# Kernel optimization log

Hardware: AMD Instinct MI355X
Metric: run time of the kernel (lower is better)

Reference implementation:

```python
import jax, jax.numpy as jnp
import numpy as np

D, H, HD, DEPTH, V, L, BOS = 128, 16, 8, 16, 17, 1024, 16

def _ln(x, s, b):
    m = jnp.mean(x, -1, keepdims=True)
    v = jnp.mean((x - m) ** 2, -1, keepdims=True)
    return (x - m) * jax.lax.rsqrt(v + 1e-5) * s + b

def _transformer(tok, emb, pos, layers, lnf_s, lnf_b, head_w, head_b):
    # tok: [B,S] int tokens. GPT-style pre-LN decoder, causal attention.
    B, S = tok.shape
    h = emb[tok] + pos[:S]
    causal = jnp.tril(jnp.ones((S, S), dtype=bool))
    inv_sqrt = np.float32(1.0 / np.sqrt(HD))
    def layer(h, p):
        ln1_s, ln1_b, wqkv, bqkv, wo, bo, ln2_s, ln2_b, w1, b1, w2, b2 = p
        x = _ln(h, ln1_s, ln1_b)
        qkv = x @ wqkv + bqkv  # [B,S,3D]
        q, k, v = jnp.split(qkv, 3, axis=-1)
        q = q.reshape(B, S, H, HD)
        k = k.reshape(B, S, H, HD)
        v = v.reshape(B, S, H, HD)
        att = jnp.einsum('bshd,bthd->bhst', q, k) * inv_sqrt
        att = jax.nn.softmax(jnp.where(causal, att, -1e9), axis=-1)
        o = jnp.einsum('bhst,bthd->bshd', att, v).reshape(B, S, D)
        h = h + o @ wo + bo
        x = _ln(h, ln2_s, ln2_b)
        h = h + jax.nn.gelu(x @ w1 + b1) @ w2 + b2
        return h, None
    h, _ = jax.lax.scan(layer, h, layers)
    return _ln(h, lnf_s, lnf_b) @ head_w + head_b  # [B,S,V]

def setup_inputs() -> dict:
    key = jax.random.key(0)
    ks = jax.random.split(key, 8)
    s = 0.02
    return {
        'tokens': jax.random.randint(ks[0], (1, L), 0, BOS, dtype=jnp.int32),
        'emb': jax.random.normal(ks[1], (V, D), jnp.float32) * s,
        'pos': jax.random.normal(ks[2], (L, D), jnp.float32) * s,
        'ln1_s': jnp.ones((DEPTH, D)), 'ln1_b': jnp.zeros((DEPTH, D)),
        'wqkv': jax.random.normal(ks[3], (DEPTH, D, 3 * D), jnp.float32) * s,
        'bqkv': jnp.zeros((DEPTH, 3 * D)),
        'wo': jax.random.normal(ks[4], (DEPTH, D, D), jnp.float32) * s,
        'bo': jnp.zeros((DEPTH, D)),
        'ln2_s': jnp.ones((DEPTH, D)), 'ln2_b': jnp.zeros((DEPTH, D)),
        'w1': jax.random.normal(ks[5], (DEPTH, D, 4 * D), jnp.float32) * s,
        'b1': jnp.zeros((DEPTH, 4 * D)),
        'w2': jax.random.normal(ks[6], (DEPTH, 4 * D, D), jnp.float32) * s,
        'b2': jnp.zeros((DEPTH, D)),
        'lnf_s': jnp.ones((D,)), 'lnf_b': jnp.zeros((D,)),
        'head_w': jax.random.normal(ks[7], (D, V), jnp.float32) * s,
        'head_b': jnp.zeros((V,)),
    }

def reference(tokens, emb, pos, ln1_s, ln1_b, wqkv, bqkv, wo, bo, ln2_s, ln2_b, w1, b1, w2, b2, lnf_s, lnf_b, head_w, head_b):
    layers = (ln1_s, ln1_b, wqkv, bqkv, wo, bo, ln2_s, ln2_b, w1, b1, w2, b2)
    tf = lambda t: _transformer(t, emb, pos, layers, lnf_s, lnf_b, head_w, head_b)
    # BOS-pad (pad value == num_embeddings == 16), as in F.pad(latent,(1,0),value=16)
    lat = jnp.concatenate([jnp.full((1, 1), BOS, jnp.int32), tokens.astype(jnp.int32)], axis=1)  # [1,1025]
    # likelihood pass: next-token log-prob of each latent token
    logits = tf(lat[:, :L])                               # [1,1024,V]
    logp = jax.nn.log_softmax(logits, axis=-1)
    ll = jnp.take_along_axis(logp, lat[:, 1:, None], axis=-1)[..., 0]  # [1,1024]
    mask = ll[0] < jnp.quantile(ll, 0.03)
    # token-healing loop: per masked position, rerun transformer, argmax (BOS excluded)
    def body(i, lat):
        def heal(lat):
            lg = tf(lat[:, :L])  # causal => position i-1 equals prefix-run logits
            row = jax.lax.dynamic_index_in_dim(lg, i - 1, axis=1, keepdims=False)[0]  # [V]
            probs = jax.nn.softmax(row).at[BOS].set(0.0)
            return lat.at[:, i].set(jnp.argmax(probs).astype(jnp.int32))
        return jax.lax.cond(mask[i - 1], heal, lambda l: l, lat)
    lat = jax.lax.fori_loop(1, L + 1, body, lat)
    out_logits = tf(lat[:, :L])  # logits over healed sequence (float output)
    return (out_logits, lat[:, 1:])
```

## Files before the change

kernel.cpp:

```cpp
#include <hip/hip_runtime.h>
#include <math.h>

#define D 128
#define NLAYER 16
#define V 17
#define L 1024
#define BOSX 16
#define NWG 256
#define NT 512

struct P {
  const int* tokens;
  const float *emb, *pos, *ln1_s, *ln1_b, *wqkv, *bqkv, *wo, *bo;
  const float *ln2_s, *ln2_b, *w1, *b1, *w2, *b2, *lnf_s, *lnf_b, *hw, *hb;
  float *kc, *vc, *ll_;
  int *lat, *heal_row, *barc, *done, *heals_done, *prog;
  float *logits, *out_tok;
};

__device__ __forceinline__ void stUf(float* p, float v) {
  __hip_atomic_store(p, v, __ATOMIC_RELAXED, __HIP_MEMORY_SCOPE_SYSTEM);
}
__device__ __forceinline__ int ldUi(const int* p) {
  return __hip_atomic_load((int*)p, __ATOMIC_RELAXED, __HIP_MEMORY_SCOPE_SYSTEM);
}
__device__ __forceinline__ void stUi(int* p, int v) {
  __hip_atomic_store(p, v, __ATOMIC_RELAXED, __HIP_MEMORY_SCOPE_SYSTEM);
}

__device__ __forceinline__ void barFull(int* cnt, int& b) {
  asm volatile("s_waitcnt vmcnt(0)" ::: "memory");
  __syncthreads();
  if (threadIdx.x == 0) {
    __threadfence();
    __hip_atomic_fetch_add(cnt, 1, __ATOMIC_RELAXED, __HIP_MEMORY_SCOPE_AGENT);
    int tgt = (b + 1) * NWG;
    while (__hip_atomic_load(cnt, __ATOMIC_RELAXED, __HIP_MEMORY_SCOPE_AGENT) < tgt)
      __builtin_amdgcn_s_sleep(8);
    __threadfence();
  }
  b += 1;
  __syncthreads();
}

__device__ __forceinline__ float geluf(float a) {
  float cgv = 0.7978845608028654f * (a + 0.044715f * a * a * a);
  cgv = fminf(fmaxf(cgv, -15.f), 15.f);
  float e = __expf(2.f * cgv);
  return 0.5f * a * (1.f + (e - 1.f) / (e + 1.f));
}

__device__ void lnorm(const float* __restrict__ s, const float* __restrict__ b,
                      const float* in, float* out, float* red) {
  int t = threadIdx.x;
  float v = (t < D) ? in[t] : 0.f;
  float sm = v;
#pragma unroll
  for (int o = 32; o; o >>= 1) sm += __shfl_xor(sm, o, 64);
  if (t < D && (t & 63) == 0) red[t >> 6] = sm;
  __syncthreads();
  float mean = (red[0] + red[1]) * (1.f / 128.f);
  float d = (t < D) ? (v - mean) : 0.f;
  float vs = d * d;
#pragma unroll
  for (int o = 32; o; o >>= 1) vs += __shfl_xor(vs, o, 64);
  if (t < D && (t & 63) == 0) red[2 + (t >> 6)] = vs;
  __syncthreads();
  float rstd = rsqrtf((red[2] + red[3]) * (1.f / 128.f) + 1e-5f);
  if (t < D) out[t] = d * rstd * s[t] + b[t];
  __syncthreads();
}

template <bool HEAL>
__device__ void qkvPub(const P& p, int l, int row, int split, const float* x, float* qrow) {
  int t = threadIdx.x;
  if (t < 384) {
    const float* w = p.wqkv + (size_t)l * D * 384 + t;
    float a = 0.f;
#pragma unroll 8
    for (int d = 0; d < D; ++d) a += x[d] * w[d * 384];
    a += p.bqkv[l * 384 + t];
    float* kcl = p.kc + (size_t)l * L * D + (size_t)row * D;
    float* vcl = p.vc + (size_t)l * L * D + (size_t)row * D;
    if (t < 128) qrow[t] = a;
    else if (t < 256) { if (HEAL) stUf(&kcl[t - 128], a); else kcl[t - 128] = a; }
    else              { if (HEAL) stUf(&vcl[t - 256], a); else vcl[t - 256] = a; }
  }
  if (HEAL) {
    asm volatile("s_waitcnt vmcnt(0)" ::: "memory");
    __syncthreads();
    if (t == 0) {
      int* dl = p.done + l * L;
      if (row - 1 >= split)
        while (ldUi(&dl[row - 1]) < 1) __builtin_amdgcn_s_sleep(1);
      stUi(&dl[row], 1);
    }
    __syncthreads();
  } else {
    __syncthreads();
  }
}

__device__ void attnProjFFN(const P& p, int row, int l,
                            float* hrow, const float* qrow,
                            float* oS, float* xnS, float* fS, float* padS, float* redS) {
  int t = threadIdx.x;
  const float* kcl = p.kc + (size_t)l * L * D;
  const float* vcl = p.vc + (size_t)l * L * D;
  int head = t >> 5, lane = t & 31;
  const float* qh = qrow + head * 8;
  float q0=qh[0],q1=qh[1],q2=qh[2],q3=qh[3],q4=qh[4],q5=qh[5],q6=qh[6],q7=qh[7];
  float sum = 0.f, a0=0,a1=0,a2=0,a3=0,a4=0,a5=0,a6=0,a7=0;
#pragma unroll 2
  for (int key = lane; key <= row; key += 32) {
    const float4* kp = (const float4*)(kcl + (size_t)key * D + head * 8);
    float4 k0 = kp[0], k1 = kp[1];
    float sc = q0*k0.x+q1*k0.y+q2*k0.z+q3*k0.w+q4*k1.x+q5*k1.y+q6*k1.z+q7*k1.w;
    float pr = __expf(sc * 0.35355339059327376f);
    const float4* vp = (const float4*)(vcl + (size_t)key * D + head * 8);
    float4 v0 = vp[0], v1 = vp[1];
    sum += pr;
    a0+=pr*v0.x; a1+=pr*v0.y; a2+=pr*v0.z; a3+=pr*v0.w;
    a4+=pr*v1.x; a5+=pr*v1.y; a6+=pr*v1.z; a7+=pr*v1.w;
  }
#pragma unroll
  for (int o = 1; o < 32; o <<= 1) {
    sum += __shfl_xor(sum, o, 32);
    a0 += __shfl_xor(a0, o, 32); a1 += __shfl_xor(a1, o, 32);
    a2 += __shfl_xor(a2, o, 32); a3 += __shfl_xor(a3, o, 32);
    a4 += __shfl_xor(a4, o, 32); a5 += __shfl_xor(a5, o, 32);
    a6 += __shfl_xor(a6, o, 32); a7 += __shfl_xor(a7, o, 32);
  }
  if (lane == 0) {
    float inv = 1.f / sum;
    oS[head*8+0]=a0*inv; oS[head*8+1]=a1*inv; oS[head*8+2]=a2*inv; oS[head*8+3]=a3*inv;
    oS[head*8+4]=a4*inv; oS[head*8+5]=a5*inv; oS[head*8+6]=a6*inv; oS[head*8+7]=a7*inv;
  }
  __syncthreads();
  {
    int col = t & 127, seg = t >> 7;
    const float* wp = p.wo + (size_t)l * D * D + col;
    float acc = 0.f;
    int d0 = seg * 32;
#pragma unroll 8
    for (int d = d0; d < d0 + 32; ++d) acc += oS[d] * wp[d * D];
    padS[t] = acc;
  }
  __syncthreads();
  if (t < D) hrow[t] += padS[t] + padS[t+128] + padS[t+256] + padS[t+384] + p.bo[l * D + t];
  __syncthreads();
  lnorm(p.ln2_s + l * D, p.ln2_b + l * D, hrow, xnS, redS);
  {
    const float* w1p = p.w1 + (size_t)l * D * 512 + t;
    float acc = 0.f;
#pragma unroll 8
    for (int d = 0; d < D; ++d) acc += xnS[d] * w1p[d * 512];
    fS[t] = geluf(acc + p.b1[l * 512 + t]);
  }
  __syncthreads();
  {
    int col = t & 127, seg = t >> 7;
    const float* w2p = p.w2 + (size_t)l * 512 * D + col;
    float acc = 0.f;
    int d0 = seg * 128;
#pragma unroll 8
    for (int d = d0; d < d0 + 128; ++d) acc += fS[d] * w2p[d * D];
    padS[t] = acc;
  }
  __syncthreads();
  if (t < D) hrow[t] += padS[t] + padS[t+128] + padS[t+256] + padS[t+384] + p.b2[l * D + t];
  __syncthreads();
}

template <bool HEAL>
__device__ void headRow(const P& p, int row, float* hrow,
                        float* xnS, float* redS, float* padS, float* oS) {
  lnorm(p.lnf_s, p.lnf_b, hrow, xnS, redS);
  int t = threadIdx.x;
  if (t < V * 8) {
    int col = t >> 3, seg = t & 7;
    float acc = 0.f;
    int d0 = seg * 16;
#pragma unroll
    for (int d = d0; d < d0 + 16; ++d) acc += xnS[d] * p.hw[d * V + col];
    padS[t] = acc;
  }
  __syncthreads();
  if (t < V) {
    float a = padS[t*8]+padS[t*8+1]+padS[t*8+2]+padS[t*8+3]
            + padS[t*8+4]+padS[t*8+5]+padS[t*8+6]+padS[t*8+7] + p.hb[t];
    oS[t] = a;
    if (HEAL) stUf(&p.logits[row * V + t], a);
    else      p.logits[row * V + t] = a;
  }
  __syncthreads();
}

__global__ void kInit(const int* __restrict__ tokens, int* __restrict__ lat,
                      int* __restrict__ barc, int* __restrict__ done,
                      int* __restrict__ hd) {
  int i = blockIdx.x * blockDim.x + threadIdx.x;
  if (i == 0) stUi(lat, BOSX);
  if (i < L) stUi(lat + i + 1, tokens[i]);
  if (i < 64) stUi(barc + i, 0);
  if (i < 16) stUi(hd + i, 0);
  if (i < NLAYER * L) stUi(done + i, 0);
}

__global__ void __launch_bounds__(NT, 1) kMega(P p) {
  __shared__ float hS[4][D];
  __shared__ float qS[4][D];
  __shared__ float xnS[D];
  __shared__ float oS[D];
  __shared__ float fS[512];
  __shared__ float padS[512];
  __shared__ float redS[16];
  __shared__ float sortS[L];
  __shared__ int cntS[NT + 1];
  int wg = blockIdx.x, t = threadIdx.x;
  int b = 0;
  int* cnt = p.barc;

  for (int i = 0; i < 4; ++i) {
    int row = wg + i * NWG;
    int tok = p.lat[row];
    if (t < D) hS[i][t] = p.emb[tok * D + t] + p.pos[row * D + t];
    __syncthreads();
    lnorm(p.ln1_s, p.ln1_b, hS[i], xnS, redS);
    qkvPub<false>(p, 0, row, 0, xnS, qS[i]);
  }
  barFull(cnt, b);
  for (int l = 0; l < NLAYER; ++l) {
    for (int i = 0; i < 4; ++i) {
      int row = wg + i * NWG;
      attnProjFFN(p, row, l, hS[i], qS[i], oS, xnS, fS, padS, redS);
      if (l < NLAYER - 1) {
        lnorm(p.ln1_s + (l+1)*D, p.ln1_b + (l+1)*D, hS[i], xnS, redS);
        qkvPub<false>(p, l + 1, row, 0, xnS, qS[i]);
      } else {
        headRow<false>(p, row, hS[i], xnS, redS, padS, oS);
      }
    }
    barFull(cnt, b);
  }

  {
    int gid = wg * NT + t;
    if (gid < L) {
      float r[V];
#pragma unroll
      for (int v = 0; v < V; ++v) r[v] = p.logits[gid * V + v];
      float m = r[0];
#pragma unroll
      for (int v = 1; v < V; ++v) m = fmaxf(m, r[v]);
      float s = 0.f;
#pragma unroll
      for (int v = 0; v < V; ++v) s += expf(r[v] - m);
      p.ll_[gid] = r[p.lat[gid + 1]] - (m + logf(s));
    }
  }
  barFull(cnt, b);

  if (wg == 0) {
    for (int i = t; i < L; i += NT) sortS[i] = p.ll_[i];
    __syncthreads();
    for (int ksz = 2; ksz <= L; ksz <<= 1) {
      for (int j = ksz >> 1; j; j >>= 1) {
        for (int i = t; i < L; i += NT) {
          int l2 = i ^ j;
          if (l2 > i) {
            bool up = ((i & ksz) == 0);
            float a = sortS[i], bb = sortS[l2];
            if ((a > bb) == up) { sortS[i] = bb; sortS[l2] = a; }
          }
        }
        __syncthreads();
      }
    }
    if (t == 0) {
      double frac = 0.03 * 1023.0 - 30.0;
      redS[0] = (float)((double)sortS[30] + frac * ((double)sortS[31] - (double)sortS[30]));
    }
    __syncthreads();
    float val = redS[0];
    float lv0 = p.ll_[t * 2], lv1 = p.ll_[t * 2 + 1];
    int loc[2], cc = 0;
    if (lv0 < val) loc[cc++] = t * 2;
    if (lv1 < val) loc[cc++] = t * 2 + 1;
    cntS[t] = cc;
    __syncthreads();
    if (t == 0) {
      int run = 0;
      for (int i = 0; i < NT; ++i) { int c2 = cntS[i]; cntS[i] = run; run += c2; }
      cntS[NT] = run;
    }
    __syncthreads();
    int base = cntS[t];
    for (int j = 0; j < cc; ++j)
      if (base + j < 31) p.heal_row[base + j] = loc[j];
    __syncthreads();
    if (t == 0) {
      int c = cntS[NT]; if (c > 31) c = 31;
      p.heal_row[31] = c;
      stUi(p.heals_done, 1);
      if (c > 0) {
        int r0 = p.heal_row[0];
        int best = 0; float bv = p.logits[r0 * V];
        for (int v = 1; v < BOSX; ++v) {
          float x = p.logits[r0 * V + v];
          if (x > bv) { bv = x; best = v; }
        }
        stUi(&p.lat[r0 + 1], best);
      }
    }
  }
  barFull(cnt, b);

  int c = p.heal_row[31];
  int split = (c > 0) ? (p.heal_row[0] + 1) : L;
  for (int r = split + wg; r < L; r += NWG) {
    int nh = 0, hk = -1;
    bool firstRow = false;
    for (int j = 0; j < c; ++j) {
      nh += (p.heal_row[j] < r) ? 1 : 0;
      if (j >= 1 && p.heal_row[j] == r) hk = j;
      if (p.heal_row[j] == r - 1) firstRow = true;
    }
    {
      int pfi = (wg * 7) % 96;
      for (;;) {
        if (t == 0) { cntS[0] = ldUi(p.heals_done); cntS[1] = ldUi(p.prog); }
        __syncthreads();
        if (cntS[0] >= nh) break;
        int pl = (cntS[1] + 1) & 15;
        float sink = 0.f;
#pragma unroll
        for (int j2 = 0; j2 < 4; ++j2) {
          int ch = pfi + j2; if (ch >= 96) ch -= 96;
          const float* basep; int off;
          if (ch < 24)      { basep = p.wqkv + (size_t)pl * D * 384; off = ch * 2048; }
          else if (ch < 32) { basep = p.wo   + (size_t)pl * D * D;   off = (ch - 24) * 2048; }
          else if (ch < 64) { basep = p.w1   + (size_t)pl * D * 512; off = (ch - 32) * 2048; }
          else              { basep = p.w2   + (size_t)pl * 512 * D; off = (ch - 64) * 2048; }
          float4 v = *(const float4*)(basep + off + t * 4);
          sink += v.x + v.y + v.z + v.w;
        }
        asm volatile("" :: "v"(sink));
        pfi += 4; if (pfi >= 96) pfi -= 96;
        __syncthreads();
      }
      if (t == 0) cntS[0] = ldUi(&p.lat[r]);
      __syncthreads();
    }
    int tok = cntS[0];
    if (t < D) hS[0][t] = p.emb[tok * D + t] + p.pos[r * D + t];
    __syncthreads();
    lnorm(p.ln1_s, p.ln1_b, hS[0], xnS, redS);
    qkvPub<true>(p, 0, r, split, xnS, qS[0]);
    for (int l = 0; l < NLAYER; ++l) {
      if (firstRow && t == 0) stUi(p.prog, l);
      attnProjFFN(p, r, l, hS[0], qS[0], oS, xnS, fS, padS, redS);
      if (l < NLAYER - 1) {
        lnorm(p.ln1_s + (l+1)*D, p.ln1_b + (l+1)*D, hS[0], xnS, redS);
        qkvPub<true>(p, l + 1, r, split, xnS, qS[0]);
      } else {
        headRow<true>(p, r, hS[0], xnS, redS, padS, oS);
      }
    }
    if (hk >= 0 && t == 0) {
      int best = 0; float bv = oS[0];
      for (int v = 1; v < BOSX; ++v)
        if (oS[v] > bv) { bv = oS[v]; best = v; }
      stUi(&p.lat[r + 1], best);
      asm volatile("s_waitcnt vmcnt(0)" ::: "memory");
      stUi(p.heals_done, hk + 1);
    }
  }

  barFull(cnt, b);

  {
    int gid = wg * NT + t;
    if (gid < L) p.out_tok[gid] = (float)ldUi(&p.lat[gid + 1]);
  }
}

extern "C" void kernel_launch(void* const* d_in, const int* in_sizes, int n_in,
                              void* d_out, int out_size, void* d_ws, size_t ws_size,
                              hipStream_t stream) {
  P prm;
  prm.tokens = (const int*)d_in[0];
  prm.emb    = (const float*)d_in[1];
  prm.pos    = (const float*)d_in[2];
  prm.ln1_s  = (const float*)d_in[3];
  prm.ln1_b  = (const float*)d_in[4];
  prm.wqkv   = (const float*)d_in[5];
  prm.bqkv   = (const float*)d_in[6];
  prm.wo     = (const float*)d_in[7];
  prm.bo     = (const float*)d_in[8];
  prm.ln2_s  = (const float*)d_in[9];
  prm.ln2_b  = (const float*)d_in[10];
  prm.w1     = (const float*)d_in[11];
  prm.b1     = (const float*)d_in[12];
  prm.w2     = (const float*)d_in[13];
  prm.b2     = (const float*)d_in[14];
  prm.lnf_s  = (const float*)d_in[15];
  prm.lnf_b  = (const float*)d_in[16];
  prm.hw     = (const float*)d_in[17];
  prm.hb     = (const float*)d_in[18];

  float* ws = (float*)d_ws;
  prm.kc   = ws;
  prm.vc   = prm.kc + (size_t)NLAYER*L*D;
  prm.ll_  = prm.vc + (size_t)NLAYER*L*D;
  prm.lat        = (int*)(prm.ll_ + L);
  prm.heal_row   = prm.lat + 1032;
  prm.barc       = prm.heal_row + 32;
  prm.done       = prm.barc + 64;
  prm.heals_done = prm.done + NLAYER * L;
  prm.prog       = prm.heals_done + 8;

  prm.logits  = (float*)d_out;
  prm.out_tok = prm.logits + L * V;

  kInit<<<64, 256, 0, stream>>>(prm.tokens, prm.lat, prm.barc, prm.done, prm.heals_done);

  void* args[] = { &prm };
  (void)hipLaunchCooperativeKernel((const void*)kMega, dim3(NWG), dim3(NT), args, 0, stream);
}
```

Measured before the change: 18.54 ms.

## Extend idle-wait prefetch to KV cache, spin-only for lead row, deeper unroll

Workgroups that are waiting on heals now also touch KV-cache blocks of the upcoming layer in their prefetch loop, in addition to the weight matrices, and prefetch six chunks per iteration instead of four. The workgroup that computes the row right after a healed position now spins with a sleep on thread 0 instead of issuing prefetch loads, so it does not contend for bandwidth on the critical path. Matvec unroll factors for the QKV, W1 and W2 loops go from 8 to 16. The goal is to keep next-layer data warm in L2 and cut latency on the serial healing chain. The cost is extra memory traffic from the waiting workgroups and higher register pressure from the deeper unrolling.

```diff
diff --git a/kernel.cpp b/kernel.cpp
--- a/kernel.cpp
+++ b/kernel.cpp
@@ -77,7 +77,7 @@
   if (t < 384) {
     const float* w = p.wqkv + (size_t)l * D * 384 + t;
     float a = 0.f;
-#pragma unroll 8
+#pragma unroll 16
     for (int d = 0; d < D; ++d) a += x[d] * w[d * 384];
     a += p.bqkv[l * 384 + t];
     float* kcl = p.kc + (size_t)l * L * D + (size_t)row * D;
@@ -153,7 +153,7 @@
   {
     const float* w1p = p.w1 + (size_t)l * D * 512 + t;
     float acc = 0.f;
-#pragma unroll 8
+#pragma unroll 16
     for (int d = 0; d < D; ++d) acc += xnS[d] * w1p[d * 512];
     fS[t] = geluf(acc + p.b1[l * 512 + t]);
   }
@@ -163,7 +163,7 @@
     const float* w2p = p.w2 + (size_t)l * 512 * D + col;
     float acc = 0.f;
     int d0 = seg * 128;
-#pragma unroll 8
+#pragma unroll 16
     for (int d = d0; d < d0 + 128; ++d) acc += fS[d] * w2p[d * D];
     padS[t] = acc;
   }
@@ -320,33 +320,49 @@
   int split = (c > 0) ? (p.heal_row[0] + 1) : L;
   for (int r = split + wg; r < L; r += NWG) {
     int nh = 0, hk = -1;
-    bool firstRow = false;
+    bool leadRow = false;
     for (int j = 0; j < c; ++j) {
       nh += (p.heal_row[j] < r) ? 1 : 0;
       if (j >= 1 && p.heal_row[j] == r) hk = j;
-      if (p.heal_row[j] == r - 1) firstRow = true;
-    }
-    {
-      int pfi = (wg * 7) % 96;
+      if (p.heal_row[j] == r - 1) leadRow = true;
+    }
+    if (leadRow) {
+      if (t == 0) {
+        while (ldUi(p.heals_done) < nh) __builtin_amdgcn_s_sleep(1);
+        cntS[0] = ldUi(&p.lat[r]);
+      }
+      __syncthreads();
+    } else {
+      int pfi = (wg * 11) % 224;
       for (;;) {
         if (t == 0) { cntS[0] = ldUi(p.heals_done); cntS[1] = ldUi(p.prog); }
         __syncthreads();
-        if (cntS[0] >= nh) break;
+        int hd = cntS[0];
+        if (hd >= nh) break;
         int pl = (cntS[1] + 1) & 15;
+        int R = p.heal_row[hd - 1];
         float sink = 0.f;
 #pragma unroll
-        for (int j2 = 0; j2 < 4; ++j2) {
-          int ch = pfi + j2; if (ch >= 96) ch -= 96;
-          const float* basep; int off;
-          if (ch < 24)      { basep = p.wqkv + (size_t)pl * D * 384; off = ch * 2048; }
-          else if (ch < 32) { basep = p.wo   + (size_t)pl * D * D;   off = (ch - 24) * 2048; }
-          else if (ch < 64) { basep = p.w1   + (size_t)pl * D * 512; off = (ch - 32) * 2048; }
-          else              { basep = p.w2   + (size_t)pl * 512 * D; off = (ch - 64) * 2048; }
-          float4 v = *(const float4*)(basep + off + t * 4);
-          sink += v.x + v.y + v.z + v.w;
+        for (int j2 = 0; j2 < 6; ++j2) {
+          int ch = pfi + j2; if (ch >= 224) ch -= 224;
+          const float* basep = nullptr;
+          if (ch < 24)      basep = p.wqkv + (size_t)pl * D * 384 + ch * 2048;
+          else if (ch < 32) basep = p.wo   + (size_t)pl * D * D   + (ch - 24) * 2048;
+          else if (ch < 64) basep = p.w1   + (size_t)pl * D * 512 + (ch - 32) * 2048;
+          else if (ch < 96) basep = p.w2   + (size_t)pl * 512 * D + (ch - 64) * 2048;
+          else {
+            int kvch = ch - 96;
+            int blk = (kvch & 63) * 16;
+            if (blk + 15 <= R)
+              basep = (kvch < 64 ? p.kc : p.vc) + (size_t)pl * L * D + (size_t)blk * D;
+          }
+          if (basep) {
+            float4 v = *(const float4*)(basep + t * 4);
+            sink += v.x + v.y + v.z + v.w;
+          }
         }
         asm volatile("" :: "v"(sink));
-        pfi += 4; if (pfi >= 96) pfi -= 96;
+        pfi += 6; if (pfi >= 224) pfi -= 224;
         __syncthreads();
       }
       if (t == 0) cntS[0] = ldUi(&p.lat[r]);
@@ -358,7 +374,7 @@
     lnorm(p.ln1_s, p.ln1_b, hS[0], xnS, redS);
     qkvPub<true>(p, 0, r, split, xnS, qS[0]);
     for (int l = 0; l < NLAYER; ++l) {
-      if (firstRow && t == 0) stUi(p.prog, l);
+      if (leadRow && t == 0) stUi(p.prog, l);
       attnProjFFN(p, r, l, hS[0], qS[0], oS, xnS, fS, padS, redS);
       if (l < NLAYER - 1) {
         lnorm(p.ln1_s + (l+1)*D, p.ln1_b + (l+1)*D, hS[0], xnS, redS);
```

Result: faster. 17.60 ms (-5.1%).
